# Optimization experiments

Hardware: AMD Instinct MI355X
Metric: run time of the kernel (lower is better)

Reference implementation:

```python
import jax, jax.numpy as jnp
import numpy as np
import math

D_MODEL = 1024
N_HEADS = 16
N_QUBITS = 8
HEAD_DIM = D_MODEL // N_HEADS
B, L = 2, 2048


def setup_inputs() -> dict:
    key = jax.random.key(0)
    ks = jax.random.split(key, 16)
    s = 0.02
    return {
        "query": jax.random.normal(ks[0], (B, L, D_MODEL), jnp.float32),
        "key_": jax.random.normal(ks[1], (B, L, D_MODEL), jnp.float32),
        "value": jax.random.normal(ks[2], (B, L, D_MODEL), jnp.float32),
        "Wq": jax.random.normal(ks[3], (D_MODEL, D_MODEL), jnp.float32) * s,
        "bq": jnp.zeros((D_MODEL,), jnp.float32),
        "Wk": jax.random.normal(ks[4], (D_MODEL, D_MODEL), jnp.float32) * s,
        "bk": jnp.zeros((D_MODEL,), jnp.float32),
        "Wv": jax.random.normal(ks[5], (D_MODEL, D_MODEL), jnp.float32) * s,
        "bv": jnp.zeros((D_MODEL,), jnp.float32),
        "Wo": jax.random.normal(ks[6], (D_MODEL, D_MODEL), jnp.float32) * s,
        "bo": jnp.zeros((D_MODEL,), jnp.float32),
        "Wf": jax.random.normal(ks[7], (HEAD_DIM, N_QUBITS), jnp.float32) * s,  # feature map weight (input->qubits)
        "bf": jnp.zeros((N_QUBITS,), jnp.float32),
        "quantum_weights": jax.random.normal(ks[8], (N_HEADS, N_QUBITS), jnp.float32) * 0.1,
        "entanglement_strength": jnp.asarray(0.5, jnp.float32),
    }


def _heads(x):
    # [B, L, D] -> [B, H, L, head_dim]
    b, l, _ = x.shape
    return x.reshape(b, l, N_HEADS, HEAD_DIM).transpose(0, 2, 1, 3)


def reference(query, key_, value, Wq, bq, Wk, bk, Wv, bv, Wo, bo, Wf, bf, quantum_weights, entanglement_strength):
    Qh = _heads(query @ Wq.T + bq)   # [B,H,L,d]
    Kh = _heads(key_ @ Wk.T + bk)
    Vh = _heads(value @ Wv.T + bv)

    classical = jnp.einsum("bhid,bhjd->bhij", Qh, Kh) / math.sqrt(HEAD_DIM)

    # quantum feature map: tanh(linear) -> [B,H,L,Q]
    qq = jnp.tanh(jnp.einsum("bhld,dq->bhlq", Qh, Wf) + bf)
    kq = jnp.tanh(jnp.einsum("bhld,dq->bhlq", Kh, Wf) + bf)

    # mean_q w_q*cos(qq_i - kq_j) == (1/Q)[(w*cos qq)@cos(kq)^T + (w*sin qq)@sin(kq)^T]
    w = jax.nn.sigmoid(quantum_weights)[None, :, None, :]  # [1,H,1,Q]
    quantum = (
        jnp.einsum("bhiq,bhjq->bhij", jnp.cos(qq) * w, jnp.cos(kq))
        + jnp.einsum("bhiq,bhjq->bhij", jnp.sin(qq) * w, jnp.sin(kq))
    ) / N_QUBITS
    ent = jax.nn.sigmoid(entanglement_strength)
    quantum = quantum * ent

    mix = ent  # same sigmoid(entanglement_strength) used as mixing weight
    combined = (1.0 - mix) * classical + mix * quantum

    attn = jax.nn.softmax(combined, axis=-1)  # [B,H,L,L]
    attended = jnp.einsum("bhij,bhjd->bhid", attn, Vh)
    attended = attended.transpose(0, 2, 1, 3).reshape(query.shape[0], query.shape[1], D_MODEL)
    output = attended @ Wo.T + bo
    return output, attn.mean(axis=1)
```

## Files before the change

kernel.cpp:

```cpp
#include <hip/hip_runtime.h>


typedef unsigned short u16;
typedef unsigned int u32;
typedef short v8s __attribute__((ext_vector_type(8)));
typedef float v4f __attribute__((ext_vector_type(4)));

static __device__ __forceinline__ float b2f(u16 h) {
  union { u32 u; float f; } a; a.u = ((u32)h) << 16; return a.f;
}
static __device__ __forceinline__ u16 f2b(float f) {
  union { float f; u32 u; } a; a.f = f;
  u32 u = a.u;
  u32 r = u + 0x7FFFu + ((u >> 16) & 1u);
  return (u16)(r >> 16);
}
static __device__ __forceinline__ u32 fbits(float f) {
  union { float f; u32 u; } a; a.f = f; return a.u;
}
static __device__ __forceinline__ v4f mfma16(v8s a, v8s b, v4f c) {
  return __builtin_amdgcn_mfma_f32_16x16x32_bf16(a, b, c, 0, 0, 0);
}
static __device__ __forceinline__ void gload16(const u16* g, u16* l) {
  __builtin_amdgcn_global_load_lds((const __attribute__((address_space(1))) u32*)g,
                                   (__attribute__((address_space(3))) u32*)l, 16, 0, 0);
}

__global__ __launch_bounds__(256) void k_f2b_all(const float* __restrict__ q, const float* __restrict__ k,
                                                 const float* __restrict__ v, const float* __restrict__ wq,
                                                 const float* __restrict__ wk, const float* __restrict__ wv,
                                                 const float* __restrict__ wo, u16* __restrict__ y) {
  int i = blockIdx.x * 256 + threadIdx.x;
  const float* src; int off;
  if (i < 1048576)      { src = q;  off = i; }
  else if (i < 2097152) { src = k;  off = i - 1048576; }
  else if (i < 3145728) { src = v;  off = i - 2097152; }
  else if (i < 3407872) { src = wq; off = i - 3145728; }
  else if (i < 3670016) { src = wk; off = i - 3407872; }
  else if (i < 3932160) { src = wv; off = i - 3670016; }
  else                  { src = wo; off = i - 3932160; }
  float4 val = ((const float4*)src)[off];
  union { u16 s[4]; uint2 u; } o;
  o.s[0] = f2b(val.x); o.s[1] = f2b(val.y); o.s[2] = f2b(val.z); o.s[3] = f2b(val.w);
  ((uint2*)y)[i] = o.u;
}

__global__ __launch_bounds__(256) void k_gemm128(
    const u16* __restrict__ A0, const u16* __restrict__ A1, const u16* __restrict__ A2,
    const u16* __restrict__ B0, const u16* __restrict__ B1, const u16* __restrict__ B2,
    const float* __restrict__ bias0, const float* __restrict__ bias1, const float* __restrict__ bias2,
    u16* __restrict__ O0, u16* __restrict__ O1, u16* __restrict__ O2t,
    float* __restrict__ Cf) {
  __shared__ __align__(16) u16 pool[18432];
  u16* As = pool;
  u16* Bs = pool + 8192;
  const int K = 1024, N = 1024;
  int t = threadIdx.x, w = t >> 6, lane = t & 63, quad = lane >> 4, l16 = lane & 15;
  int z = blockIdx.z;
  const u16* A = (z == 0) ? A0 : (z == 1) ? A1 : A2;
  const u16* Bm = (z == 0) ? B0 : (z == 1) ? B1 : B2;
  const float* bias = (z == 0) ? bias0 : (z == 1) ? bias1 : bias2;
  int n0 = blockIdx.x * 128, m0 = blockIdx.y * 128;

  int srow = lane >> 2, scol = (lane & 3) * 8;
  const u16* gp[8]; u16* lp[8];
#pragma unroll
  for (int qi = 0; qi < 8; ++qi) {
    int mat = qi >> 2, kk = (qi >> 1) & 1, g = w + (qi & 1) * 4;
    int row = g * 16 + srow;
    gp[qi] = (mat ? Bm + (size_t)(n0 + row) * K : A + (size_t)(m0 + row) * K) + kk * 32 + scol;
    lp[qi] = (mat ? Bs : As) + kk * 4096 + g * 512;
  }

  int mrow = (w >> 1) * 64, ncol = (w & 1) * 64;
  v4f zf = {0.f, 0.f, 0.f, 0.f};
  v4f acc[4][4];
#pragma unroll
  for (int mi = 0; mi < 4; ++mi)
#pragma unroll
    for (int ni = 0; ni < 4; ++ni) acc[mi][ni] = zf;

  for (int k0 = 0; k0 < K; k0 += 64) {
    __syncthreads();
#pragma unroll
    for (int qi = 0; qi < 8; ++qi) gload16(gp[qi] + k0, lp[qi]);
    __syncthreads();
#pragma unroll
    for (int kk = 0; kk < 2; ++kk) {
      v8s af[4], bfr[4];
#pragma unroll
      for (int x = 0; x < 4; ++x) {
        af[x] = *(const v8s*)&As[kk * 4096 + (mrow + x * 16 + l16) * 32 + quad * 8];
        bfr[x] = *(const v8s*)&Bs[kk * 4096 + (ncol + x * 16 + l16) * 32 + quad * 8];
      }
#pragma unroll
      for (int mi = 0; mi < 4; ++mi)
#pragma unroll
        for (int ni = 0; ni < 4; ++ni)
          acc[mi][ni] = mfma16(af[mi], bfr[ni], acc[mi][ni]);
    }
  }

  float bv[4];
#pragma unroll
  for (int ni = 0; ni < 4; ++ni) bv[ni] = bias[n0 + ncol + ni * 16 + l16];

  if (Cf) {
#pragma unroll
    for (int mi = 0; mi < 4; ++mi)
#pragma unroll
      for (int ni = 0; ni < 4; ++ni)
#pragma unroll
        for (int r = 0; r < 4; ++r)
          Cf[(size_t)(m0 + mrow + mi * 16 + quad * 4 + r) * N + n0 + ncol + ni * 16 + l16] =
              acc[mi][ni][r] + bv[ni];
  } else if (z != 2) {
    u16* O = z ? O1 : O0;
#pragma unroll
    for (int mi = 0; mi < 4; ++mi)
#pragma unroll
      for (int ni = 0; ni < 4; ++ni)
#pragma unroll
        for (int r = 0; r < 4; ++r)
          O[(size_t)(m0 + mrow + mi * 16 + quad * 4 + r) * N + n0 + ncol + ni * 16 + l16] =
              f2b(acc[mi][ni][r] + bv[ni]);
  } else {
    __syncthreads();
    u16* Ts = pool + w * 64 * 68;
#pragma unroll
    for (int mi = 0; mi < 4; ++mi)
#pragma unroll
      for (int ni = 0; ni < 4; ++ni)
#pragma unroll
        for (int r = 0; r < 4; ++r)
          Ts[(mi * 16 + quad * 4 + r) * 68 + ni * 16 + l16] = f2b(acc[mi][ni][r] + bv[ni]);
    int c = lane;
    union { uint4 u[8]; u16 s[64]; } cb;
#pragma unroll
    for (int e = 0; e < 64; ++e) cb.s[e] = Ts[e * 68 + c];
    int bb = m0 >> 11, ml = m0 & 2047;
    u16* dst = O2t + ((size_t)(bb * 1024 + n0 + ncol + c)) * 2048 + ml + mrow;
#pragma unroll
    for (int e = 0; e < 8; ++e) *(uint4*)(dst + e * 8) = cb.u[e];
  }
}

__global__ __launch_bounds__(256) void k_features(const u16* __restrict__ Qp, const u16* __restrict__ Kp,
                                                  const float* __restrict__ Wf, const float* __restrict__ bff,
                                                  const float* __restrict__ qw, const float* __restrict__ entp,
                                                  u16* __restrict__ Qaa, u16* __restrict__ Kaa) {
  int isK = blockIdx.y;
  const u16* P = isK ? Kp : Qp;
  u16* Out = isK ? Kaa : Qaa;
  int idx = blockIdx.x * 256 + threadIdx.x;
  int b = idx >> 15, h = (idx >> 11) & 15, l = idx & 2047;
  const u16* src = P + ((size_t)(b * 2048 + l)) * 1024 + h * 64;
  u16* dst = Out + (size_t)idx * 96;
  const float4* Wf4 = (const float4*)Wf;

  float x[64];
#pragma unroll
  for (int g = 0; g < 8; ++g) {
    union { uint4 u; u16 s[8]; } uu;
    uu.u = *(const uint4*)(src + g * 8);
#pragma unroll
    for (int e = 0; e < 8; ++e) x[g * 8 + e] = b2f(uu.s[e]);
  }
  float qv[8];
#pragma unroll
  for (int qq = 0; qq < 8; ++qq) qv[qq] = bff[qq];
#pragma unroll
  for (int d = 0; d < 64; ++d) {
    float4 wa = Wf4[d * 2], wb = Wf4[d * 2 + 1];
    float xd = x[d];
    qv[0] += xd * wa.x; qv[1] += xd * wa.y; qv[2] += xd * wa.z; qv[3] += xd * wa.w;
    qv[4] += xd * wb.x; qv[5] += xd * wb.y; qv[6] += xd * wb.z; qv[7] += xd * wb.w;
  }
  float cs[8], sn[8];
#pragma unroll
  for (int qq = 0; qq < 8; ++qq) {
    float e2 = __expf(2.f * qv[qq]);
    float th = 1.f - 2.f / (e2 + 1.f);
    __sincosf(th, &sn[qq], &cs[qq]);
  }
  float ent = 1.f / (1.f + __expf(-entp[0]));
  union { uint4 u; u16 s[8]; } pc, ps;
  if (!isK) {
#pragma unroll
    for (int g = 0; g < 8; ++g) *(uint4*)(dst + g * 8) = *(const uint4*)(src + g * 8);
#pragma unroll
    for (int qq = 0; qq < 8; ++qq) {
      float sw = 1.f / (1.f + __expf(-qw[h * 8 + qq]));
      pc.s[qq] = f2b(cs[qq] * sw);
      ps.s[qq] = f2b(sn[qq] * sw);
    }
  } else {
    float c1 = (1.f - ent) * 0.125f, c2 = ent * ent * 0.125f;
#pragma unroll
    for (int g = 0; g < 8; ++g) {
      union { uint4 u; u16 s[8]; } ob;
#pragma unroll
      for (int e = 0; e < 8; ++e) ob.s[e] = f2b(x[g * 8 + e] * c1);
      *(uint4*)(dst + g * 8) = ob.u;
    }
#pragma unroll
    for (int qq = 0; qq < 8; ++qq) {
      pc.s[qq] = f2b(cs[qq] * c2);
      ps.s[qq] = f2b(sn[qq] * c2);
    }
  }
  *(uint4*)(dst + 64) = pc.u;
  *(uint4*)(dst + 72) = ps.u;
  uint4 z4 = {0, 0, 0, 0};
  *(uint4*)(dst + 80) = z4;
  *(uint4*)(dst + 88) = z4;
}

__global__ __launch_bounds__(256) void k_flash(const u16* __restrict__ Qa, const u16* __restrict__ Ka,
                                               const u16* __restrict__ VtG, u16* __restrict__ At,
                                               float* __restrict__ lb) {
  __shared__ __align__(16) u16 Ks[2][64][104];
  __shared__ __align__(16) u16 Ps[4][2][16][72];

  int t = threadIdx.x, w = t >> 6, lane = t & 63, quad = lane >> 4, l16 = lane & 15;
  int i0 = blockIdx.x * 128, h = blockIdx.y, b = blockIdx.z;
  size_t qbase = ((size_t)(b * 16 + h)) * 2048 * 96;
  v8s aq[2][3];
#pragma unroll
  for (int i16 = 0; i16 < 2; ++i16) {
    const u16* Qrow = Qa + qbase + (size_t)(i0 + w * 32 + i16 * 16 + l16) * 96;
#pragma unroll
    for (int ks = 0; ks < 3; ++ks) aq[i16][ks] = *(const v8s*)(Qrow + ks * 32 + quad * 8);
  }
  const u16* Kbase = Ka + qbase;
  const u16* Vbase = VtG + ((size_t)(b * 1024 + h * 64)) * 2048;

  const u16* kg[3]; int kdo[3];
#pragma unroll
  for (int p = 0; p < 3; ++p) {
    int idx = t + p * 256, r_ = idx / 12, c_ = idx % 12;
    kg[p] = Kbase + (size_t)r_ * 96 + c_ * 8;
    kdo[p] = r_ * 104 + c_ * 8;
  }
  u16* ks0 = &Ks[0][0][0];
  u16* ks1 = &Ks[1][0][0];

  v4f zf = {0.f, 0.f, 0.f, 0.f};
  v4f oacc[2][4];
#pragma unroll
  for (int i16 = 0; i16 < 2; ++i16)
#pragma unroll
    for (int d16 = 0; d16 < 4; ++d16) oacc[i16][d16] = zf;
  float l_acc[2] = {0.f, 0.f};

  uint4 fk0 = *(const uint4*)kg[0];
  uint4 fk1 = *(const uint4*)kg[1];
  uint4 fk2 = *(const uint4*)kg[2];
  kg[0] += 6144; kg[1] += 6144; kg[2] += 6144;
  *(uint4*)(ks0 + kdo[0]) = fk0;
  *(uint4*)(ks0 + kdo[1]) = fk1;
  *(uint4*)(ks0 + kdo[2]) = fk2;
  fk0 = *(const uint4*)kg[0];
  fk1 = *(const uint4*)kg[1];
  fk2 = *(const uint4*)kg[2];
  kg[0] += 6144; kg[1] += 6144; kg[2] += 6144;
  v8s vf[8];
#pragma unroll
  for (int idx = 0; idx < 8; ++idx)
    vf[idx] = *(const v8s*)(Vbase + (size_t)((idx >> 1) * 16 + l16) * 2048 + (idx & 1) * 32 + quad * 8);
  __syncthreads();

  for (int j0 = 0; j0 < 2048; j0 += 64) {
    int cur = (j0 >> 6) & 1;
    const u16* kb = cur ? ks1 : ks0;
    u16* kw = cur ? ks0 : ks1;
    bool more = (j0 + 64) < 2048;
    if (more) {
      *(uint4*)(kw + kdo[0]) = fk0;
      *(uint4*)(kw + kdo[1]) = fk1;
      *(uint4*)(kw + kdo[2]) = fk2;
    }
    if (j0 + 128 < 2048) {
      fk0 = *(const uint4*)kg[0];
      fk1 = *(const uint4*)kg[1];
      fk2 = *(const uint4*)kg[2];
      kg[0] += 6144; kg[1] += 6144; kg[2] += 6144;
    }
    v8s vn[8];
    if (more) {
#pragma unroll
      for (int idx = 0; idx < 8; ++idx)
        vn[idx] = *(const v8s*)(Vbase + (size_t)((idx >> 1) * 16 + l16) * 2048 + j0 + 64 +
                                (idx & 1) * 32 + quad * 8);
    }

    v4f sacc[2][4];
#pragma unroll
    for (int i16 = 0; i16 < 2; ++i16)
#pragma unroll
      for (int j16 = 0; j16 < 4; ++j16) sacc[i16][j16] = zf;
#pragma unroll
    for (int j16 = 0; j16 < 4; ++j16)
#pragma unroll
      for (int ks = 0; ks < 3; ++ks) {
        v8s kf = *(const v8s*)(kb + (j16 * 16 + l16) * 104 + ks * 32 + quad * 8);
        sacc[0][j16] = mfma16(kf, aq[0][ks], sacc[0][j16]);
        sacc[1][j16] = mfma16(kf, aq[1][ks], sacc[1][j16]);
      }

#pragma unroll
    for (int i16 = 0; i16 < 2; ++i16)
#pragma unroll
      for (int j16 = 0; j16 < 4; ++j16) {
        float e0 = __expf(sacc[i16][j16][0]);
        float e1 = __expf(sacc[i16][j16][1]);
        float e2 = __expf(sacc[i16][j16][2]);
        float e3 = __expf(sacc[i16][j16][3]);
        l_acc[i16] += (e0 + e1) + (e2 + e3);
        uint2 pp;
        pp.x = __builtin_amdgcn_perm(fbits(e1) + 0x8000u, fbits(e0) + 0x8000u, 0x07060302u);
        pp.y = __builtin_amdgcn_perm(fbits(e3) + 0x8000u, fbits(e2) + 0x8000u, 0x07060302u);
        *(uint2*)&Ps[w][i16][l16][j16 * 16 + quad * 4] = pp;
      }
#pragma unroll
    for (int jh = 0; jh < 2; ++jh) {
      v8s pf0 = *(const v8s*)&Ps[w][0][l16][jh * 32 + quad * 8];
      v8s pf1 = *(const v8s*)&Ps[w][1][l16][jh * 32 + quad * 8];
#pragma unroll
      for (int d16 = 0; d16 < 4; ++d16) {
        v8s vv = vf[d16 * 2 + jh];
        oacc[0][d16] = mfma16(pf0, vv, oacc[0][d16]);
        oacc[1][d16] = mfma16(pf1, vv, oacc[1][d16]);
      }
    }
    if (more) {
#pragma unroll
      for (int idx = 0; idx < 8; ++idx) vf[idx] = vn[idx];
      __syncthreads();
    }
  }

#pragma unroll
  for (int i16 = 0; i16 < 2; ++i16) {
    l_acc[i16] += __shfl_xor(l_acc[i16], 16, 64);
    l_acc[i16] += __shfl_xor(l_acc[i16], 32, 64);
    float linv = 1.f / l_acc[i16];
#pragma unroll
    for (int r = 0; r < 4; ++r) {
      float li = __shfl(linv, quad * 4 + r, 64);
      int ri = i0 + w * 32 + i16 * 16 + quad * 4 + r;
#pragma unroll
      for (int d16 = 0; d16 < 4; ++d16)
        At[((size_t)(b * 2048 + ri)) * 1024 + h * 64 + d16 * 16 + l16] = f2b(oacc[i16][d16][r] * li);
    }
    if (lane < 16) {
      size_t mbase = ((size_t)(b * 16 + h)) * 2048;
      lb[mbase + i0 + w * 32 + i16 * 16 + lane] = l_acc[i16];
    }
  }
}

__global__ __launch_bounds__(256) void k_pass2(const u16* __restrict__ Qa, const u16* __restrict__ Ka,
                                               const float* __restrict__ lb,
                                               float* __restrict__ out1) {
  __shared__ __align__(16) u16 Ks[64][104];
  __shared__ float Ls[16][128];
  int t = threadIdx.x, w = t >> 6, lane = t & 63, quad = lane >> 4, l16 = lane & 15;
  int j0 = blockIdx.x * 64, i0 = blockIdx.y * 128, b = blockIdx.z;

#pragma unroll
  for (int rep = 0; rep < 8; ++rep) {
    int idx = t + rep * 256;
    int hh = idx >> 7, il = idx & 127;
    Ls[hh][il] = 0.0625f / lb[((size_t)(b * 16 + hh)) * 2048 + i0 + il];
  }

  size_t base0 = (size_t)b * 16 * 2048 * 96;
  const u16* kg[3]; u16* kd[3];
#pragma unroll
  for (int rep = 0; rep < 3; ++rep) {
    int idx = t + rep * 256;
    int r_ = idx / 12, c_ = idx % 12;
    kg[rep] = Ka + base0 + (size_t)(j0 + r_) * 96 + c_ * 8;
    kd[rep] = &Ks[r_][c_ * 8];
  }
  uint4 f0 = *(const uint4*)kg[0];
  uint4 f1 = *(const uint4*)kg[1];
  uint4 f2 = *(const uint4*)kg[2];

  const u16* q0 = Qa + base0 + (size_t)(i0 + w * 32 + l16) * 96 + quad * 8;
  const u16* q1 = q0 + 16 * 96;

  v4f zf = {0.f, 0.f, 0.f, 0.f};
  v4f macc[2][4];
#pragma unroll
  for (int i16 = 0; i16 < 2; ++i16)
#pragma unroll
    for (int j16 = 0; j16 < 4; ++j16) macc[i16][j16] = zf;

  v8s a[2][3];
#pragma unroll
  for (int ks = 0; ks < 3; ++ks) {
    a[0][ks] = *(const v8s*)(q0 + ks * 32);
    a[1][ks] = *(const v8s*)(q1 + ks * 32);
  }

  for (int h = 0; h < 16; ++h) {
    *(uint4*)kd[0] = f0;
    *(uint4*)kd[1] = f1;
    *(uint4*)kd[2] = f2;
    __syncthreads();
    if (h < 15) {
      kg[0] += 196608; kg[1] += 196608; kg[2] += 196608;
      f0 = *(const uint4*)kg[0];
      f1 = *(const uint4*)kg[1];
      f2 = *(const uint4*)kg[2];
    }

    v4f sacc[2][4];
#pragma unroll
    for (int i16 = 0; i16 < 2; ++i16)
#pragma unroll
      for (int j16 = 0; j16 < 4; ++j16) sacc[i16][j16] = zf;
#pragma unroll
    for (int ks = 0; ks < 3; ++ks)
#pragma unroll
      for (int j16 = 0; j16 < 4; ++j16) {
        v8s kf = *(const v8s*)&Ks[j16 * 16 + l16][ks * 32 + quad * 8];
        sacc[0][j16] = mfma16(a[0][ks], kf, sacc[0][j16]);
        sacc[1][j16] = mfma16(a[1][ks], kf, sacc[1][j16]);
      }

    if (h < 15) {
      q0 += 196608; q1 += 196608;
#pragma unroll
      for (int ks = 0; ks < 3; ++ks) {
        a[0][ks] = *(const v8s*)(q0 + ks * 32);
        a[1][ks] = *(const v8s*)(q1 + ks * 32);
      }
    }

    float li[2][4];
#pragma unroll
    for (int i16 = 0; i16 < 2; ++i16)
#pragma unroll
      for (int r = 0; r < 4; ++r)
        li[i16][r] = Ls[h][w * 32 + i16 * 16 + quad * 4 + r];
#pragma unroll
    for (int i16 = 0; i16 < 2; ++i16)
#pragma unroll
      for (int j16 = 0; j16 < 4; ++j16)
#pragma unroll
        for (int r = 0; r < 4; ++r)
          macc[i16][j16][r] += __expf(sacc[i16][j16][r]) * li[i16][r];
    __syncthreads();
  }

  float* o = out1 + (size_t)b * 2048 * 2048;
#pragma unroll
  for (int i16 = 0; i16 < 2; ++i16)
#pragma unroll
    for (int j16 = 0; j16 < 4; ++j16)
#pragma unroll
      for (int r = 0; r < 4; ++r)
        o[(size_t)(i0 + w * 32 + i16 * 16 + quad * 4 + r) * 2048 + j0 + j16 * 16 + l16] =
            macc[i16][j16][r];
}

extern "C" void kernel_launch(void* const* d_in, const int* in_sizes, int n_in,
                              void* d_out, int out_size, void* d_ws, size_t ws_size,
                              hipStream_t stream) {
  (void)in_sizes; (void)n_in; (void)out_size; (void)ws_size;
  const float* query = (const float*)d_in[0];
  const float* key_  = (const float*)d_in[1];
  const float* value = (const float*)d_in[2];
  const float* Wq = (const float*)d_in[3];
  const float* bq = (const float*)d_in[4];
  const float* Wk = (const float*)d_in[5];
  const float* bk = (const float*)d_in[6];
  const float* Wv = (const float*)d_in[7];
  const float* bv = (const float*)d_in[8];
  const float* Wo = (const float*)d_in[9];
  const float* bo = (const float*)d_in[10];
  const float* Wf = (const float*)d_in[11];
  const float* bff = (const float*)d_in[12];
  const float* qw = (const float*)d_in[13];
  const float* entp = (const float*)d_in[14];

  char* p = (char*)d_ws;
  u16* Xq  = (u16*)(p + 0);
  u16* Xk  = (u16*)(p + 8388608);
  u16* Xv  = (u16*)(p + 16777216);
  u16* Wqb = (u16*)(p + 25165824);
  u16* Wkb = (u16*)(p + 27262976);
  u16* Wvb = (u16*)(p + 29360128);
  u16* Qp  = (u16*)(p + 33554432);
  u16* Kp  = (u16*)(p + 41943040);
  u16* VtG = (u16*)(p + 50331648);
  u16* Qaa = (u16*)(p + 58720256);
  u16* Kaa = (u16*)(p + 71303168);
  float* lb = (float*)(p + 84148224);
  u16* At  = (u16*)(p + 84410368);
  u16* Wob = (u16*)(p + 31457280);

  k_f2b_all<<<16384, 256, 0, stream>>>(query, key_, value, Wq, Wk, Wv, Wo, Xq);

  k_gemm128<<<dim3(8, 32, 3), 256, 0, stream>>>(Xq, Xk, Xv, Wqb, Wkb, Wvb, bq, bk, bv,
                                                Qp, Kp, VtG, nullptr);

  k_features<<<dim3(256, 2), 256, 0, stream>>>(Qp, Kp, Wf, bff, qw, entp, Qaa, Kaa);

  k_flash<<<dim3(16, 16, 2), 256, 0, stream>>>(Qaa, Kaa, VtG, At, lb);

  k_pass2<<<dim3(32, 16, 2), 256, 0, stream>>>(Qaa, Kaa, lb, (float*)d_out + 4194304);

  k_gemm128<<<dim3(8, 32, 1), 256, 0, stream>>>(At, At, At, Wob, Wob, Wob, bo, bo, bo,
                                                nullptr, nullptr, nullptr, (float*)d_out);
}
```

Measured before the change: 350.5 us.

## Use native exp2 with folded log2e, hardware bf16 pack, XCD-aware block mapping, MFMA priority

Folds log2(e) into the K-side scaling so the flash and pass-2 kernels can call the raw v_exp_f32 instruction instead of __expf. Replaces the manual bf16 rounding via perm with the v_cvt_pk_bf16_f32 instruction. Remaps 1D block IDs so blocks sharing the same head and batch land on the same XCD, improving L2 reuse of K and V. Raises wave priority around the MFMA sections to favour matrix work. Risks include small numeric differences from the new rounding path and reliance on the mapping matching the XCD round-robin dispatch.

```diff
diff --git a/kernel.cpp b/kernel.cpp
--- a/kernel.cpp
+++ b/kernel.cpp
@@ -15,15 +15,18 @@
   u32 r = u + 0x7FFFu + ((u >> 16) & 1u);
   return (u16)(r >> 16);
 }
-static __device__ __forceinline__ u32 fbits(float f) {
-  union { float f; u32 u; } a; a.f = f; return a.u;
-}
 static __device__ __forceinline__ v4f mfma16(v8s a, v8s b, v4f c) {
   return __builtin_amdgcn_mfma_f32_16x16x32_bf16(a, b, c, 0, 0, 0);
 }
 static __device__ __forceinline__ void gload16(const u16* g, u16* l) {
   __builtin_amdgcn_global_load_lds((const __attribute__((address_space(1))) u32*)g,
                                    (__attribute__((address_space(3))) u32*)l, 16, 0, 0);
+}
+static __device__ __forceinline__ float exp2fast(float x) {
+  float r; asm("v_exp_f32 %0, %1" : "=v"(r) : "v"(x)); return r;
+}
+static __device__ __forceinline__ u32 cvtpk_bf16(float lo, float hi) {
+  u32 r; asm("v_cvt_pk_bf16_f32 %0, %1, %2" : "=v"(r) : "v"(lo), "v"(hi)); return r;
 }
 
 __global__ __launch_bounds__(256) void k_f2b_all(const float* __restrict__ q, const float* __restrict__ k,
@@ -195,7 +198,8 @@
       ps.s[qq] = f2b(sn[qq] * sw);
     }
   } else {
-    float c1 = (1.f - ent) * 0.125f, c2 = ent * ent * 0.125f;
+    const float LOG2E = 1.44269504088896f;
+    float c1 = (1.f - ent) * 0.125f * LOG2E, c2 = ent * ent * 0.125f * LOG2E;
 #pragma unroll
     for (int g = 0; g < 8; ++g) {
       union { uint4 u; u16 s[8]; } ob;
@@ -223,7 +227,11 @@
   __shared__ __align__(16) u16 Ps[4][2][16][72];
 
   int t = threadIdx.x, w = t >> 6, lane = t & 63, quad = lane >> 4, l16 = lane & 15;
-  int i0 = blockIdx.x * 128, h = blockIdx.y, b = blockIdx.z;
+  int bid = blockIdx.x;
+  int sem = ((bid & 7) << 6) | (bid >> 3);
+  int i0 = (sem & 15) << 7;
+  int hb = sem >> 4;
+  int h = hb & 15, b = hb >> 4;
   size_t qbase = ((size_t)(b * 16 + h)) * 2048 * 96;
   v8s aq[2][3];
 #pragma unroll
@@ -299,6 +307,7 @@
     for (int i16 = 0; i16 < 2; ++i16)
 #pragma unroll
       for (int j16 = 0; j16 < 4; ++j16) sacc[i16][j16] = zf;
+    __builtin_amdgcn_s_setprio(1);
 #pragma unroll
     for (int j16 = 0; j16 < 4; ++j16)
 #pragma unroll
@@ -307,21 +316,24 @@
         sacc[0][j16] = mfma16(kf, aq[0][ks], sacc[0][j16]);
         sacc[1][j16] = mfma16(kf, aq[1][ks], sacc[1][j16]);
       }
+    __builtin_amdgcn_s_setprio(0);
 
 #pragma unroll
     for (int i16 = 0; i16 < 2; ++i16)
 #pragma unroll
       for (int j16 = 0; j16 < 4; ++j16) {
-        float e0 = __expf(sacc[i16][j16][0]);
-        float e1 = __expf(sacc[i16][j16][1]);
-        float e2 = __expf(sacc[i16][j16][2]);
-        float e3 = __expf(sacc[i16][j16][3]);
+        float e0 = exp2fast(sacc[i16][j16][0]);
+        float e1 = exp2fast(sacc[i16][j16][1]);
+        float e2 = exp2fast(sacc[i16][j16][2]);
+        float e3 = exp2fast(sacc[i16][j16][3]);
         l_acc[i16] += (e0 + e1) + (e2 + e3);
         uint2 pp;
-        pp.x = __builtin_amdgcn_perm(fbits(e1) + 0x8000u, fbits(e0) + 0x8000u, 0x07060302u);
-        pp.y = __builtin_amdgcn_perm(fbits(e3) + 0x8000u, fbits(e2) + 0x8000u, 0x07060302u);
+        pp.x = cvtpk_bf16(e0, e1);
+        pp.y = cvtpk_bf16(e2, e3);
         *(uint2*)&Ps[w][i16][l16][j16 * 16 + quad * 4] = pp;
       }
+
+    __builtin_amdgcn_s_setprio(1);
 #pragma unroll
     for (int jh = 0; jh < 2; ++jh) {
       v8s pf0 = *(const v8s*)&Ps[w][0][l16][jh * 32 + quad * 8];
@@ -333,6 +345,7 @@
         oacc[1][d16] = mfma16(pf1, vv, oacc[1][d16]);
       }
     }
+    __builtin_amdgcn_s_setprio(0);
     if (more) {
 #pragma unroll
       for (int idx = 0; idx < 8; ++idx) vf[idx] = vn[idx];
@@ -366,7 +379,12 @@
   __shared__ __align__(16) u16 Ks[64][104];
   __shared__ float Ls[16][128];
   int t = threadIdx.x, w = t >> 6, lane = t & 63, quad = lane >> 4, l16 = lane & 15;
-  int j0 = blockIdx.x * 64, i0 = blockIdx.y * 128, b = blockIdx.z;
+  int bid = blockIdx.x;
+  int sem = ((bid & 7) << 7) | (bid >> 3);
+  int xcd = sem >> 7;
+  int b = xcd >> 2;
+  int i0 = ((((xcd & 3) << 2) | (sem & 3))) << 7;
+  int j0 = ((sem >> 2) & 31) << 6;
 
 #pragma unroll
   for (int rep = 0; rep < 8; ++rep) {
@@ -452,7 +470,7 @@
       for (int j16 = 0; j16 < 4; ++j16)
 #pragma unroll
         for (int r = 0; r < 4; ++r)
-          macc[i16][j16][r] += __expf(sacc[i16][j16][r]) * li[i16][r];
+          macc[i16][j16][r] += exp2fast(sacc[i16][j16][r]) * li[i16][r];
     __syncthreads();
   }
 
@@ -510,9 +528,9 @@
 
   k_features<<<dim3(256, 2), 256, 0, stream>>>(Qp, Kp, Wf, bff, qw, entp, Qaa, Kaa);
 
-  k_flash<<<dim3(16, 16, 2), 256, 0, stream>>>(Qaa, Kaa, VtG, At, lb);
-
-  k_pass2<<<dim3(32, 16, 2), 256, 0, stream>>>(Qaa, Kaa, lb, (float*)d_out + 4194304);
+  k_flash<<<dim3(512), 256, 0, stream>>>(Qaa, Kaa, VtG, At, lb);
+
+  k_pass2<<<dim3(1024), 256, 0, stream>>>(Qaa, Kaa, lb, (float*)d_out + 4194304);
 
   k_gemm128<<<dim3(8, 32, 1), 256, 0, stream>>>(At, At, At, Wob, Wob, Wob, bo, bo, bo,
                                                 nullptr, nullptr, nullptr, (float*)d_out);
```

After: 349.1 us. Within noise of the previous version (-0.4%).
